# Kernel tuning notes

Hardware: AMD Instinct MI355X
Metric: run time of the kernel (lower is better)

## Reference

```python
import jax, jax.numpy as jnp
import numpy as np

B, C, H, W = 8, 512, 64, 64
IC = C // 2  # inter_channel


def setup_inputs() -> dict:
    key = jax.random.key(0)
    ks = jax.random.split(key, 10)
    s = 0.02
    return {
        "x": jax.random.normal(ks[0], (B, C, H, W), dtype=jnp.float32),
        "y": jax.random.normal(ks[1], (B, C, H, W), dtype=jnp.float32),
        "w_phi": jax.random.normal(ks[2], (IC, C), dtype=jnp.float32) * s,
        "b_phi": jnp.zeros((IC,), dtype=jnp.float32),
        "w_theta": jax.random.normal(ks[3], (IC, C), dtype=jnp.float32) * s,
        "b_theta": jnp.zeros((IC,), dtype=jnp.float32),
        "w_g": jax.random.normal(ks[4], (IC, C), dtype=jnp.float32) * s,
        "b_g": jnp.zeros((IC,), dtype=jnp.float32),
        "w_mask": jax.random.normal(ks[5], (C, IC), dtype=jnp.float32) * s,
        "b_mask": jnp.zeros((C,), dtype=jnp.float32),
    }


def _conv1x1(w, b, t):
    # t: [b, cin, h, w]; 1x1 conv == channel matmul
    return jnp.einsum('oc,bchw->bohw', w, t) + b[None, :, None, None]


def reference(x, y, w_phi, b_phi, w_theta, b_theta, w_g, b_g, w_mask, b_mask):
    b, c, h, w = x.shape
    ic = w_phi.shape[0]  # c // 2
    # Faithful to the torch code: conv outputs ic channels but is viewed as
    # (b, c, -1), so the sequence length is N = h*w//2 and feature dim is c.
    x_phi = _conv1x1(w_phi, b_phi, y).reshape(b, c, -1)              # [b, c, N]
    x_theta = _conv1x1(w_theta, b_theta, x).reshape(b, c, -1)
    x_theta = jnp.transpose(x_theta, (0, 2, 1))                      # [b, N, c]
    x_g = _conv1x1(w_g, b_g, x).reshape(b, c, -1)
    dict
    x_g = jnp.transpose(x_g, (0, 2, 1))                              # [b, N, c]
    scores = jnp.einsum('bnc,bcm->bnm', x_theta, x_phi)              # [b, N, N]
    attn = jax.nn.softmax(scores, axis=1)  # softmax over dim=1 (columns), as in torch
    out_nl = jnp.einsum('bnm,bmc->bnc', attn, x_g)                   # [b, N, c]
    out_nl = jnp.transpose(out_nl, (0, 2, 1)).reshape(b, ic, h, w)   # [b, ic, h, w]
    mask = _conv1x1(w_mask, b_mask, out_nl)                          # [b, c, h, w]
    return mask + x
```

## Files before the change

### kernel.cpp

```cpp
#include <hip/hip_runtime.h>
#include <hip/hip_bf16.h>


typedef __attribute__((ext_vector_type(8))) short short8;
typedef __attribute__((ext_vector_type(4))) short short4v;
typedef __attribute__((ext_vector_type(4))) float f32x4;

__device__ __forceinline__ short f2bf(float f) {
  union { __hip_bfloat16 h; short s; } u; u.h = __float2bfloat16(f); return u.s;
}
__device__ __forceinline__ float bf2f(short s) {
  union { short s; __hip_bfloat16 h; } u; u.s = s; return __bfloat162float(u.h);
}

__device__ __forceinline__ void async_ld16(const void* g, void* l) {
  __builtin_amdgcn_global_load_lds(
      (const __attribute__((address_space(1))) unsigned int*)(unsigned long long)g,
      (__attribute__((address_space(3))) unsigned int*)(unsigned int)(unsigned long long)l,
      16, 0, 0);
}

__device__ __forceinline__ short8 frag_sw(const short* Ds, int row, int q8)
{
  return *(const short8*)&Ds[row * 32 + (((q8 >> 3) ^ ((row >> 2) & 3)) << 3)];
}

__global__ __launch_bounds__(512, 4)
void ov_k(const short* __restrict__ Eg, const short* __restrict__ Gg,
          short* __restrict__ Cg)
{
  const int L = blockIdx.x;
  const int xcd = L & 7, k = L >> 3;
  const int slab = xcd + ((k >> 2) << 3);
  const int bz = slab >> 4, by = slab & 15, bx = k & 3;

  __shared__ __align__(16) short As[128 * 32];
  __shared__ __align__(16) short Bs[128 * 32];
  const short* A = Eg + ((long)bz << 22);
  const short* B = Gg + ((long)bz << 20);
  const int m0 = by * 128;
  const int n0 = bx * 128;
  const int t = threadIdx.x;
  const int wv = t >> 6, ln = t & 63;
  const int wr = wv >> 1, wc = wv & 1;
  const int fr = ln & 15, q8 = (ln >> 4) * 8;
  const int rowA = t >> 2, kc = (t & 3) * 8;

  f32x4 acc[2][4];
  #pragma unroll
  for (int i = 0; i < 2; i++)
    #pragma unroll
    for (int j = 0; j < 4; j++)
      #pragma unroll
      for (int r = 0; r < 4; r++) acc[i][j][r] = 0.f;

  for (int kk = 0; kk < 2048; kk += 32) {
    async_ld16(A + (long)(m0 + rowA) * 2048 + kk + kc, As + wv * 512);
    async_ld16(B + (long)(n0 + rowA) * 2048 + kk + kc, Bs + wv * 512);
    __syncthreads();
    short8 af[2], bfr[4];
    #pragma unroll
    for (int mi = 0; mi < 2; mi++) af[mi] = *(const short8*)&As[(wr * 32 + mi * 16 + fr) * 32 + q8];
    #pragma unroll
    for (int ni = 0; ni < 4; ni++) bfr[ni] = *(const short8*)&Bs[(wc * 64 + ni * 16 + fr) * 32 + q8];
    #pragma unroll
    for (int mi = 0; mi < 2; mi++)
      #pragma unroll
      for (int ni = 0; ni < 4; ni++)
        acc[mi][ni] = __builtin_amdgcn_mfma_f32_16x16x32_bf16(af[mi], bfr[ni], acc[mi][ni], 0, 0, 0);
    __syncthreads();
  }

  const int colb = n0 + wc * 64 + fr;
  const int rowb = m0 + wr * 32 + (ln >> 4) * 4;
  #pragma unroll
  for (int mi = 0; mi < 2; mi++)
    #pragma unroll
    for (int r = 0; r < 4; r++) {
      const int mr = rowb + mi * 16 + r;
      #pragma unroll
      for (int ni = 0; ni < 4; ni++)
        Cg[((long)bz << 20) + (long)mr * 512 + colb + ni * 16] = f2bf(acc[mi][ni][r]);
    }
}

__global__ __launch_bounds__(512, 4)
void conv_ptf(const float* __restrict__ x, const float* __restrict__ y,
              const short* __restrict__ wth, const short* __restrict__ wph,
              const float* __restrict__ bth, const float* __restrict__ bph,
              short* __restrict__ TPT2)
{
  __shared__ __align__(16) short As[2][128 * 32];
  __shared__ __align__(16) short Bs[2][256 * 32];
  const int slab = blockIdx.x;
  const bool isphi = slab >= 256;
  const int s2 = slab & 255;
  const float* src = (isphi ? y : x) + (long)(s2 >> 5) * (512L * 4096);
  const int px0 = (s2 & 31) * 128;
  const long m0 = (long)slab * 128;
  const short* W = isphi ? wph : wth;
  const float* bias = isphi ? bph : bth;
  const int t = threadIdx.x;
  const int wv = t >> 6, ln = t & 63;
  const int wpx = wv >> 2, wic = wv & 3;
  const int fr = ln & 15, q8 = (ln >> 4) * 8;
  const int g4 = (t >> 5) * 4, p4 = (t & 31) * 4;
  const int w2 = wv - 4;

  f32x4 acc[4][4];
  #pragma unroll
  for (int i = 0; i < 4; i++)
    #pragma unroll
    for (int j = 0; j < 4; j++)
      #pragma unroll
      for (int r = 0; r < 4; r++) acc[i][j][r] = 0.f;

  if (t >= 256) {
    #pragma unroll
    for (int j = 0; j < 4; j++)
      async_ld16(W + (long)(w2 * 64 + j * 16 + (ln >> 2)) * 512 + (ln & 3) * 8,
                 &Bs[0][(w2 * 64 + j * 16) * 32]);
  } else {
    f32x4 r[4];
    #pragma unroll
    for (int i = 0; i < 4; i++)
      r[i] = *(const f32x4*)&src[(long)(g4 + i) * 4096 + px0 + p4];
    #pragma unroll
    for (int j = 0; j < 4; j++) {
      short4v w;
      w[0] = f2bf(r[0][j]); w[1] = f2bf(r[1][j]); w[2] = f2bf(r[2][j]); w[3] = f2bf(r[3][j]);
      const int px = p4 + j;
      const int u = (g4 >> 3) ^ ((px >> 2) & 3);
      *(short4v*)&As[0][px * 32 + u * 8 + (g4 & 4)] = w;
    }
  }
  __syncthreads();

  for (int k = 1; k < 16; k++) {
    const int cur = (k - 1) & 1, nxt = k & 1;
    f32x4 r[4];
    if (t >= 256) {
      #pragma unroll
      for (int j = 0; j < 4; j++)
        async_ld16(W + (long)(w2 * 64 + j * 16 + (ln >> 2)) * 512 + k * 32 + (ln & 3) * 8,
                   &Bs[nxt][(w2 * 64 + j * 16) * 32]);
    } else {
      #pragma unroll
      for (int i = 0; i < 4; i++)
        r[i] = *(const f32x4*)&src[(long)(k * 32 + g4 + i) * 4096 + px0 + p4];
    }
    short8 af[4], bfv[4];
    #pragma unroll
    for (int mi = 0; mi < 4; mi++) af[mi] = frag_sw(&As[cur][0], wpx * 64 + mi * 16 + fr, q8);
    #pragma unroll
    for (int ni = 0; ni < 4; ni++) bfv[ni] = *(const short8*)&Bs[cur][(wic * 64 + ni * 16 + fr) * 32 + q8];
    #pragma unroll
    for (int mi = 0; mi < 4; mi++)
      #pragma unroll
      for (int ni = 0; ni < 4; ni++)
        acc[mi][ni] = __builtin_amdgcn_mfma_f32_16x16x32_bf16(af[mi], bfv[ni], acc[mi][ni], 0, 0, 0);
    if (t < 256) {
      #pragma unroll
      for (int j = 0; j < 4; j++) {
        short4v w;
        w[0] = f2bf(r[0][j]); w[1] = f2bf(r[1][j]); w[2] = f2bf(r[2][j]); w[3] = f2bf(r[3][j]);
        const int px = p4 + j;
        const int u = (g4 >> 3) ^ ((px >> 2) & 3);
        *(short4v*)&As[nxt][px * 32 + u * 8 + (g4 & 4)] = w;
      }
    }
    __syncthreads();
  }

  {
    short8 af[4], bfv[4];
    #pragma unroll
    for (int mi = 0; mi < 4; mi++) af[mi] = frag_sw(&As[1][0], wpx * 64 + mi * 16 + fr, q8);
    #pragma unroll
    for (int ni = 0; ni < 4; ni++) bfv[ni] = *(const short8*)&Bs[1][(wic * 64 + ni * 16 + fr) * 32 + q8];
    #pragma unroll
    for (int mi = 0; mi < 4; mi++)
      #pragma unroll
      for (int ni = 0; ni < 4; ni++)
        acc[mi][ni] = __builtin_amdgcn_mfma_f32_16x16x32_bf16(af[mi], bfv[ni], acc[mi][ni], 0, 0, 0);
  }

  const int colic = wic * 64 + fr;
  float cb[4];
  #pragma unroll
  for (int ni = 0; ni < 4; ni++) cb[ni] = bias[colic + ni * 16];
  #pragma unroll
  for (int mi = 0; mi < 4; mi++)
    #pragma unroll
    for (int r = 0; r < 4; r++) {
      const long m = m0 + wpx * 64 + mi * 16 + (ln >> 4) * 4 + r;
      #pragma unroll
      for (int ni = 0; ni < 4; ni++)
        TPT2[m * 256 + colic + ni * 16] = f2bf(acc[mi][ni][r] + cb[ni]);
    }
}

__global__ __launch_bounds__(512, 4)
void gemmG_f(const float* __restrict__ x, const short* __restrict__ wg,
             const float* __restrict__ bg, short* __restrict__ G)
{
  __shared__ __align__(16) short As[2][256 * 32];
  __shared__ __align__(16) short Bs[2][128 * 32];
  const int img = blockIdx.y;
  const int n0 = blockIdx.x * 128;
  const float* src = x + (long)img * 512 * 4096;
  const int t = threadIdx.x;
  const int wv = t >> 6, ln = t & 63;
  const int wr = wv >> 1, wc = wv & 1;
  const int fr = ln & 15, q8 = (ln >> 4) * 8;
  const int g4 = (t >> 5) * 4, p4 = (t & 31) * 4;
  const int w2 = wv - 4;

  f32x4 acc[4][4];
  #pragma unroll
  for (int i = 0; i < 4; i++)
    #pragma unroll
    for (int j = 0; j < 4; j++)
      #pragma unroll
      for (int r = 0; r < 4; r++) acc[i][j][r] = 0.f;

  if (t >= 256) {
    #pragma unroll
    for (int j = 0; j < 4; j++)
      async_ld16(wg + (long)(w2 * 64 + j * 16 + (ln >> 2)) * 512 + (ln & 3) * 8,
                 &As[0][(w2 * 64 + j * 16) * 32]);
  } else {
    f32x4 r[4];
    #pragma unroll
    for (int i = 0; i < 4; i++)
      r[i] = *(const f32x4*)&src[(long)(g4 + i) * 4096 + n0 + p4];
    #pragma unroll
    for (int j = 0; j < 4; j++) {
      short4v w;
      w[0] = f2bf(r[0][j]); w[1] = f2bf(r[1][j]); w[2] = f2bf(r[2][j]); w[3] = f2bf(r[3][j]);
      const int px = p4 + j;
      const int u = (g4 >> 3) ^ ((px >> 2) & 3);
      *(short4v*)&Bs[0][px * 32 + u * 8 + (g4 & 4)] = w;
    }
  }
  __syncthreads();

  for (int k = 1; k < 16; k++) {
    const int cur = (k - 1) & 1, nxt = k & 1;
    f32x4 r[4];
    if (t >= 256) {
      #pragma unroll
      for (int j = 0; j < 4; j++)
        async_ld16(wg + (long)(w2 * 64 + j * 16 + (ln >> 2)) * 512 + k * 32 + (ln & 3) * 8,
                   &As[nxt][(w2 * 64 + j * 16) * 32]);
    } else {
      #pragma unroll
      for (int i = 0; i < 4; i++)
        r[i] = *(const f32x4*)&src[(long)(k * 32 + g4 + i) * 4096 + n0 + p4];
    }
    short8 af[4], bfv[4];
    #pragma unroll
    for (int mi = 0; mi < 4; mi++) af[mi] = *(const short8*)&As[cur][(wr * 64 + mi * 16 + fr) * 32 + q8];
    #pragma unroll
    for (int ni = 0; ni < 4; ni++) bfv[ni] = frag_sw(&Bs[cur][0], wc * 64 + ni * 16 + fr, q8);
    #pragma unroll
    for (int mi = 0; mi < 4; mi++)
      #pragma unroll
      for (int ni = 0; ni < 4; ni++)
        acc[mi][ni] = __builtin_amdgcn_mfma_f32_16x16x32_bf16(af[mi], bfv[ni], acc[mi][ni], 0, 0, 0);
    if (t < 256) {
      #pragma unroll
      for (int j = 0; j < 4; j++) {
        short4v w;
        w[0] = f2bf(r[0][j]); w[1] = f2bf(r[1][j]); w[2] = f2bf(r[2][j]); w[3] = f2bf(r[3][j]);
        const int px = p4 + j;
        const int u = (g4 >> 3) ^ ((px >> 2) & 3);
        *(short4v*)&Bs[nxt][px * 32 + u * 8 + (g4 & 4)] = w;
      }
    }
    __syncthreads();
  }

  {
    short8 af[4], bfv[4];
    #pragma unroll
    for (int mi = 0; mi < 4; mi++) af[mi] = *(const short8*)&As[1][(wr * 64 + mi * 16 + fr) * 32 + q8];
    #pragma unroll
    for (int ni = 0; ni < 4; ni++) bfv[ni] = frag_sw(&Bs[1][0], wc * 64 + ni * 16 + fr, q8);
    #pragma unroll
    for (int mi = 0; mi < 4; mi++)
      #pragma unroll
      for (int ni = 0; ni < 4; ni++)
        acc[mi][ni] = __builtin_amdgcn_mfma_f32_16x16x32_bf16(af[mi], bfv[ni], acc[mi][ni], 0, 0, 0);
  }

  const int colb = n0 + wc * 64 + fr;
  const int rowb = wr * 64 + (ln >> 4) * 4;
  #pragma unroll
  for (int mi = 0; mi < 4; mi++)
    #pragma unroll
    for (int r = 0; r < 4; r++) {
      const int mr = rowb + mi * 16 + r;
      const float badd = bg[mr];
      #pragma unroll
      for (int ni = 0; ni < 4; ni++)
        G[((long)img << 20) + (long)mr * 4096 + colb + ni * 16] = f2bf(acc[mi][ni][r] + badd);
    }
}

__global__ __launch_bounds__(256)
void scores_k(const short* __restrict__ TT2, const short* __restrict__ PT2,
              short* __restrict__ ST, float* __restrict__ pstats)
{
  __shared__ __align__(16) short As[128 * 32];
  __shared__ __align__(16) short Bs[128 * 32];
  const int bz = blockIdx.z, by = blockIdx.y, bx = blockIdx.x;
  const int t = threadIdx.x;
  const int wv = t >> 6, ln = t & 63;
  const int wm = (wv >> 1) * 64, wn = (wv & 1) * 64;
  const int fr = ln & 15, q8 = (ln >> 4) * 8;
  const int rowA = t >> 2, kc = (t & 3) * 8;

  f32x4 acc[4][4];
  #pragma unroll
  for (int i = 0; i < 4; i++)
    #pragma unroll
    for (int j = 0; j < 4; j++)
      #pragma unroll
      for (int r = 0; r < 4; r++) acc[i][j][r] = 0.f;

  #pragma unroll
  for (int h = 0; h < 2; h++) {
    const short* Aseg = TT2 + ((long)(bz * 4096 + h * 2048 + by * 128)) * 256;
    const short* Bseg = PT2 + ((long)(bz * 4096 + h * 2048 + bx * 128)) * 256;
    for (int kk = 0; kk < 256; kk += 32) {
      #pragma unroll
      for (int s = 0; s < 2; s++) {
        async_ld16(Aseg + (long)(s * 64 + rowA) * 256 + kk + kc, As + (s * 256 + wv * 64) * 8);
        async_ld16(Bseg + (long)(s * 64 + rowA) * 256 + kk + kc, Bs + (s * 256 + wv * 64) * 8);
      }
      __syncthreads();
      short8 af[4], bfr[4];
      #pragma unroll
      for (int mi = 0; mi < 4; mi++) af[mi] = *(const short8*)&As[(wm + mi * 16 + fr) * 32 + q8];
      #pragma unroll
      for (int ni = 0; ni < 4; ni++) bfr[ni] = *(const short8*)&Bs[(wn + ni * 16 + fr) * 32 + q8];
      #pragma unroll
      for (int mi = 0; mi < 4; mi++)
        #pragma unroll
        for (int ni = 0; ni < 4; ni++)
          acc[mi][ni] = __builtin_amdgcn_mfma_f32_16x16x32_bf16(af[mi], bfr[ni], acc[mi][ni], 0, 0, 0);
      __syncthreads();
    }
  }

  const int colb = bx * 128 + wn + fr;
  const int rowb = by * 128 + wm + (ln >> 4) * 4;
  short* base = ST + ((long)bz << 22);
  float ps[4] = {0.f, 0.f, 0.f, 0.f};
  #pragma unroll
  for (int mi = 0; mi < 4; mi++)
    #pragma unroll
    for (int r = 0; r < 4; r++) {
      const long mr = rowb + mi * 16 + r;
      #pragma unroll
      for (int ni = 0; ni < 4; ni++) {
        float e = __expf(acc[mi][ni][r]);
        base[mr * 2048 + colb + ni * 16] = f2bf(e);
        ps[ni] += e;
      }
    }
  #pragma unroll
  for (int ni = 0; ni < 4; ni++) {
    ps[ni] += __shfl_xor(ps[ni], 16);
    ps[ni] += __shfl_xor(ps[ni], 32);
  }
  float* part = (float*)As;
  if (ln < 16) {
    #pragma unroll
    for (int ni = 0; ni < 4; ni++)
      part[(wv >> 1) * 128 + wn + ni * 16 + fr] = ps[ni];
  }
  __syncthreads();
  if (t < 128)
    pstats[((long)(bz * 16 + by)) * 2048 + bx * 128 + t] = part[t] + part[128 + t];
}

__global__ __launch_bounds__(256)
void zfinal(const float* __restrict__ pstats, float* __restrict__ invZ)
{
  const int g = blockIdx.x * 256 + threadIdx.x;
  const int b = g >> 11, col = g & 2047;
  float S = 0.f;
  #pragma unroll
  for (int rc = 0; rc < 16; rc++) S += pstats[((long)(b * 16 + rc)) * 2048 + col];
  invZ[g] = 1.f / S;
}

__global__ __launch_bounds__(256)
void g_scale(short* __restrict__ G, const float* __restrict__ invZ)
{
  const long base = ((long)blockIdx.x * 256 + threadIdx.x) * 8;
  const int bz = (int)(base >> 20);
  const int n2 = (int)(base & 4095);
  const float* z = invZ + bz * 2048 + (n2 & 2047);
  short8 v = *(short8*)&G[base];
  f32x4 z0 = *(const f32x4*)z;
  f32x4 z1 = *(const f32x4*)(z + 4);
  #pragma unroll
  for (int j = 0; j < 4; j++) { v[j] = f2bf(bf2f(v[j]) * z0[j]); v[4 + j] = f2bf(bf2f(v[4 + j]) * z1[j]); }
  *(short8*)&G[base] = v;
}

__global__ __launch_bounds__(256)
void mask_k(const short* __restrict__ Wm20, const short* __restrict__ Wm21,
            const short* __restrict__ OVT, const float* __restrict__ bmask,
            const float* __restrict__ x, float* __restrict__ out)
{
  __shared__ __align__(16) short As[128 * 32];
  __shared__ __align__(16) short Bs[128 * 32];
  const int bz = blockIdx.z;
  const int n0 = blockIdx.x * 128;
  const int m0 = blockIdx.y * 128;
  const short* A = (n0 >= 2048) ? Wm21 : Wm20;
  const short* B = OVT + ((long)bz << 20) + (long)(n0 & 2047) * 512;
  const int t = threadIdx.x;
  const int wv = t >> 6, ln = t & 63;
  const int wm = (wv >> 1) * 64, wn = (wv & 1) * 64;
  const int fr = ln & 15, q8 = (ln >> 4) * 8;
  const int rowA = t >> 2, kc = (t & 3) * 8;

  f32x4 acc[4][4];
  #pragma unroll
  for (int i = 0; i < 4; i++)
    #pragma unroll
    for (int j = 0; j < 4; j++)
      #pragma unroll
      for (int r = 0; r < 4; r++) acc[i][j][r] = 0.f;

  for (int kk = 0; kk < 512; kk += 32) {
    #pragma unroll
    for (int s = 0; s < 2; s++) {
      async_ld16(A + (long)(m0 + s * 64 + rowA) * 512 + kk + kc, As + (s * 256 + wv * 64) * 8);
      async_ld16(B + (long)(s * 64 + rowA) * 512 + kk + kc, Bs + (s * 256 + wv * 64) * 8);
    }
    __syncthreads();
    short8 af[4], bfr[4];
    #pragma unroll
    for (int mi = 0; mi < 4; mi++) af[mi] = *(const short8*)&As[(wm + mi * 16 + fr) * 32 + q8];
    #pragma unroll
    for (int ni = 0; ni < 4; ni++) bfr[ni] = *(const short8*)&Bs[(wn + ni * 16 + fr) * 32 + q8];
    #pragma unroll
    for (int mi = 0; mi < 4; mi++)
      #pragma unroll
      for (int ni = 0; ni < 4; ni++)
        acc[mi][ni] = __builtin_amdgcn_mfma_f32_16x16x32_bf16(af[mi], bfr[ni], acc[mi][ni], 0, 0, 0);
    __syncthreads();
  }

  const int colb = n0 + wn + fr;
  const int rowb = m0 + wm + (ln >> 4) * 4;
  #pragma unroll
  for (int mi = 0; mi < 4; mi++)
    #pragma unroll
    for (int r = 0; r < 4; r++) {
      const int mr = rowb + mi * 16 + r;
      const float badd = bmask[mr];
      const long rbase = ((long)bz * 512 + mr) * 4096;
      #pragma unroll
      for (int ni = 0; ni < 4; ni++) {
        const int cc = colb + ni * 16;
        out[rbase + cc] = acc[mi][ni][r] + badd + x[rbase + cc];
      }
    }
}

__global__ __launch_bounds__(256)
void wconv2(const float* w_phi, const float* w_theta, const float* w_g,
            const float* w_mask,
            short* wph, short* wth, short* wg, short* Wm20, short* Wm21)
{
  const int seg = blockIdx.x >> 6;
  const int blk = blockIdx.x & 63;
  const int i0 = blk * 2048 + threadIdx.x * 8;
  if (seg < 3) {
    const float* s = seg == 0 ? w_phi : seg == 1 ? w_theta : w_g;
    short* d = seg == 0 ? wph : seg == 1 ? wth : wg;
    f32x4 a = *(const f32x4*)&s[i0];
    f32x4 b = *(const f32x4*)&s[i0 + 4];
    short8 o;
    #pragma unroll
    for (int j = 0; j < 4; j++) { o[j] = f2bf(a[j]); o[4 + j] = f2bf(b[j]); }
    *(short8*)&d[i0] = o;
  } else {
    const int o = i0 >> 8;
    f32x4 a = *(const f32x4*)&w_mask[i0];
    f32x4 b = *(const f32x4*)&w_mask[i0 + 4];
    short v[8];
    #pragma unroll
    for (int j = 0; j < 4; j++) { v[j] = f2bf(a[j]); v[4 + j] = f2bf(b[j]); }
    short8 a0, a1, b0, b1;
    #pragma unroll
    for (int j = 0; j < 4; j++) {
      a0[2 * j] = v[j];     a0[2 * j + 1] = 0;
      a1[2 * j] = v[4 + j]; a1[2 * j + 1] = 0;
      b0[2 * j] = 0;        b0[2 * j + 1] = v[j];
      b1[2 * j] = 0;        b1[2 * j + 1] = v[4 + j];
    }
    const long base = (long)o * 512 + 2 * (i0 & 255);
    *(short8*)&Wm20[base] = a0; *(short8*)&Wm20[base + 8] = a1;
    *(short8*)&Wm21[base] = b0; *(short8*)&Wm21[base + 8] = b1;
  }
}

extern "C" void kernel_launch(void* const* d_in, const int* in_sizes, int n_in,
                              void* d_out, int out_size, void* d_ws, size_t ws_size,
                              hipStream_t stream)
{
  (void)in_sizes; (void)n_in; (void)out_size; (void)ws_size;
  const float* x       = (const float*)d_in[0];
  const float* y       = (const float*)d_in[1];
  const float* w_phi   = (const float*)d_in[2];
  const float* b_phi   = (const float*)d_in[3];
  const float* w_theta = (const float*)d_in[4];
  const float* b_theta = (const float*)d_in[5];
  const float* w_g     = (const float*)d_in[6];
  const float* b_g     = (const float*)d_in[7];
  const float* w_mask  = (const float*)d_in[8];
  const float* b_mask  = (const float*)d_in[9];
  float* out = (float*)d_out;

  char* ws = (char*)d_ws;
  const long MB = 1L << 20;
  short* wph  = (short*)(ws + 0);
  short* wth  = (short*)(ws + 256 * 1024);
  short* wg   = (short*)(ws + 512 * 1024);
  short* Wm20 = (short*)(ws + 768 * 1024);
  short* Wm21 = (short*)(ws + 1280 * 1024);
  short* TPT2 = (short*)(ws + 66 * MB);
  short* G    = (short*)(ws + 98 * MB);
  short* ST   = (short*)(ws + 2 * MB);
  float* pstats = (float*)(ws + 114 * MB);
  float* invZ   = (float*)(ws + 115 * MB);
  short* OVT  = (short*)(ws + 66 * MB);

  dim3 blk(256, 1, 1);
  dim3 blk8(512, 1, 1);

  wconv2<<<dim3(256, 1, 1), blk, 0, stream>>>(w_phi, w_theta, w_g, w_mask,
                                              wph, wth, wg, Wm20, Wm21);

  conv_ptf<<<dim3(512, 1, 1), blk8, 0, stream>>>(x, y, wth, wph, b_theta, b_phi, TPT2);

  gemmG_f<<<dim3(32, 8, 1), blk8, 0, stream>>>(x, wg, b_g, G);

  scores_k<<<dim3(16, 16, 8), blk, 0, stream>>>(TPT2, TPT2 + 32768L * 256, ST, pstats);
  zfinal<<<dim3(64, 1, 1), blk, 0, stream>>>(pstats, invZ);
  g_scale<<<dim3(4096, 1, 1), blk, 0, stream>>>(G, invZ);

  ov_k<<<dim3(512, 1, 1), blk8, 0, stream>>>(ST, G, OVT);

  mask_k<<<dim3(32, 4, 8), blk, 0, stream>>>(Wm20, Wm21, OVT, b_mask, x, out);
}
```

Baseline: 358.2 us.

## Double-buffer async LDS loads and XOR-swizzle shared-memory tiles across GEMM kernels

Converts the ov_k, scores_k and mask_k main loops from single-buffered load-sync-compute-sync into double-buffered pipelines. The next tile's global_load_lds is issued while MFMAs consume the current tile, which removes one barrier per iteration. It also applies an XOR swizzle to the k-chunk offset on every async LDS load, and reads fragments through frag_sw, to cut LDS bank conflicts, including in the conv/gemmG weight tiles. The cost is twice the LDS footprint in three kernels, which may lower occupancy.

```diff
diff --git a/kernel.cpp b/kernel.cpp
--- a/kernel.cpp
+++ b/kernel.cpp
@@ -34,8 +34,8 @@
   const int slab = xcd + ((k >> 2) << 3);
   const int bz = slab >> 4, by = slab & 15, bx = k & 3;
 
-  __shared__ __align__(16) short As[128 * 32];
-  __shared__ __align__(16) short Bs[128 * 32];
+  __shared__ __align__(16) short As[2][128 * 32];
+  __shared__ __align__(16) short Bs[2][128 * 32];
   const short* A = Eg + ((long)bz << 22);
   const short* B = Gg + ((long)bz << 20);
   const int m0 = by * 128;
@@ -44,7 +44,8 @@
   const int wv = t >> 6, ln = t & 63;
   const int wr = wv >> 1, wc = wv & 1;
   const int fr = ln & 15, q8 = (ln >> 4) * 8;
-  const int rowA = t >> 2, kc = (t & 3) * 8;
+  const int rowA = t >> 2;
+  const int kcs = ((t & 3) ^ ((t >> 4) & 3)) * 8;
 
   f32x4 acc[2][4];
   #pragma unroll
@@ -54,21 +55,37 @@
       #pragma unroll
       for (int r = 0; r < 4; r++) acc[i][j][r] = 0.f;
 
-  for (int kk = 0; kk < 2048; kk += 32) {
-    async_ld16(A + (long)(m0 + rowA) * 2048 + kk + kc, As + wv * 512);
-    async_ld16(B + (long)(n0 + rowA) * 2048 + kk + kc, Bs + wv * 512);
-    __syncthreads();
+  async_ld16(A + (long)(m0 + rowA) * 2048 + kcs, &As[0][0] + wv * 512);
+  async_ld16(B + (long)(n0 + rowA) * 2048 + kcs, &Bs[0][0] + wv * 512);
+  __syncthreads();
+
+  for (int kt = 1; kt < 64; kt++) {
+    const int cur = (kt - 1) & 1, nxt = kt & 1;
+    async_ld16(A + (long)(m0 + rowA) * 2048 + kt * 32 + kcs, &As[nxt][0] + wv * 512);
+    async_ld16(B + (long)(n0 + rowA) * 2048 + kt * 32 + kcs, &Bs[nxt][0] + wv * 512);
     short8 af[2], bfr[4];
     #pragma unroll
-    for (int mi = 0; mi < 2; mi++) af[mi] = *(const short8*)&As[(wr * 32 + mi * 16 + fr) * 32 + q8];
-    #pragma unroll
-    for (int ni = 0; ni < 4; ni++) bfr[ni] = *(const short8*)&Bs[(wc * 64 + ni * 16 + fr) * 32 + q8];
+    for (int mi = 0; mi < 2; mi++) af[mi] = frag_sw(&As[cur][0], wr * 32 + mi * 16 + fr, q8);
+    #pragma unroll
+    for (int ni = 0; ni < 4; ni++) bfr[ni] = frag_sw(&Bs[cur][0], wc * 64 + ni * 16 + fr, q8);
     #pragma unroll
     for (int mi = 0; mi < 2; mi++)
       #pragma unroll
       for (int ni = 0; ni < 4; ni++)
         acc[mi][ni] = __builtin_amdgcn_mfma_f32_16x16x32_bf16(af[mi], bfr[ni], acc[mi][ni], 0, 0, 0);
     __syncthreads();
+  }
+  {
+    short8 af[2], bfr[4];
+    #pragma unroll
+    for (int mi = 0; mi < 2; mi++) af[mi] = frag_sw(&As[1][0], wr * 32 + mi * 16 + fr, q8);
+    #pragma unroll
+    for (int ni = 0; ni < 4; ni++) bfr[ni] = frag_sw(&Bs[1][0], wc * 64 + ni * 16 + fr, q8);
+    #pragma unroll
+    for (int mi = 0; mi < 2; mi++)
+      #pragma unroll
+      for (int ni = 0; ni < 4; ni++)
+        acc[mi][ni] = __builtin_amdgcn_mfma_f32_16x16x32_bf16(af[mi], bfr[ni], acc[mi][ni], 0, 0, 0);
   }
 
   const int colb = n0 + wc * 64 + fr;
@@ -106,6 +123,7 @@
   const int fr = ln & 15, q8 = (ln >> 4) * 8;
   const int g4 = (t >> 5) * 4, p4 = (t & 31) * 4;
   const int w2 = wv - 4;
+  const int kcs = ((ln & 3) ^ (ln >> 4)) * 8;
 
   f32x4 acc[4][4];
   #pragma unroll
@@ -118,7 +136,7 @@
   if (t >= 256) {
     #pragma unroll
     for (int j = 0; j < 4; j++)
-      async_ld16(W + (long)(w2 * 64 + j * 16 + (ln >> 2)) * 512 + (ln & 3) * 8,
+      async_ld16(W + (long)(w2 * 64 + j * 16 + (ln >> 2)) * 512 + kcs,
                  &Bs[0][(w2 * 64 + j * 16) * 32]);
   } else {
     f32x4 r[4];
@@ -142,7 +160,7 @@
     if (t >= 256) {
       #pragma unroll
       for (int j = 0; j < 4; j++)
-        async_ld16(W + (long)(w2 * 64 + j * 16 + (ln >> 2)) * 512 + k * 32 + (ln & 3) * 8,
+        async_ld16(W + (long)(w2 * 64 + j * 16 + (ln >> 2)) * 512 + k * 32 + kcs,
                    &Bs[nxt][(w2 * 64 + j * 16) * 32]);
     } else {
       #pragma unroll
@@ -153,7 +171,7 @@
     #pragma unroll
     for (int mi = 0; mi < 4; mi++) af[mi] = frag_sw(&As[cur][0], wpx * 64 + mi * 16 + fr, q8);
     #pragma unroll
-    for (int ni = 0; ni < 4; ni++) bfv[ni] = *(const short8*)&Bs[cur][(wic * 64 + ni * 16 + fr) * 32 + q8];
+    for (int ni = 0; ni < 4; ni++) bfv[ni] = frag_sw(&Bs[cur][0], wic * 64 + ni * 16 + fr, q8);
     #pragma unroll
     for (int mi = 0; mi < 4; mi++)
       #pragma unroll
@@ -177,7 +195,7 @@
     #pragma unroll
     for (int mi = 0; mi < 4; mi++) af[mi] = frag_sw(&As[1][0], wpx * 64 + mi * 16 + fr, q8);
     #pragma unroll
-    for (int ni = 0; ni < 4; ni++) bfv[ni] = *(const short8*)&Bs[1][(wic * 64 + ni * 16 + fr) * 32 + q8];
+    for (int ni = 0; ni < 4; ni++) bfv[ni] = frag_sw(&Bs[1][0], wic * 64 + ni * 16 + fr, q8);
     #pragma unroll
     for (int mi = 0; mi < 4; mi++)
       #pragma unroll
@@ -215,6 +233,7 @@
   const int fr = ln & 15, q8 = (ln >> 4) * 8;
   const int g4 = (t >> 5) * 4, p4 = (t & 31) * 4;
   const int w2 = wv - 4;
+  const int kcs = ((ln & 3) ^ (ln >> 4)) * 8;
 
   f32x4 acc[4][4];
   #pragma unroll
@@ -227,7 +246,7 @@
   if (t >= 256) {
     #pragma unroll
     for (int j = 0; j < 4; j++)
-      async_ld16(wg + (long)(w2 * 64 + j * 16 + (ln >> 2)) * 512 + (ln & 3) * 8,
+      async_ld16(wg + (long)(w2 * 64 + j * 16 + (ln >> 2)) * 512 + kcs,
                  &As[0][(w2 * 64 + j * 16) * 32]);
   } else {
     f32x4 r[4];
@@ -251,7 +270,7 @@
     if (t >= 256) {
       #pragma unroll
       for (int j = 0; j < 4; j++)
-        async_ld16(wg + (long)(w2 * 64 + j * 16 + (ln >> 2)) * 512 + k * 32 + (ln & 3) * 8,
+        async_ld16(wg + (long)(w2 * 64 + j * 16 + (ln >> 2)) * 512 + k * 32 + kcs,
                    &As[nxt][(w2 * 64 + j * 16) * 32]);
     } else {
       #pragma unroll
@@ -260,7 +279,7 @@
     }
     short8 af[4], bfv[4];
     #pragma unroll
-    for (int mi = 0; mi < 4; mi++) af[mi] = *(const short8*)&As[cur][(wr * 64 + mi * 16 + fr) * 32 + q8];
+    for (int mi = 0; mi < 4; mi++) af[mi] = frag_sw(&As[cur][0], wr * 64 + mi * 16 + fr, q8);
     #pragma unroll
     for (int ni = 0; ni < 4; ni++) bfv[ni] = frag_sw(&Bs[cur][0], wc * 64 + ni * 16 + fr, q8);
     #pragma unroll
@@ -284,7 +303,7 @@
   {
     short8 af[4], bfv[4];
     #pragma unroll
-    for (int mi = 0; mi < 4; mi++) af[mi] = *(const short8*)&As[1][(wr * 64 + mi * 16 + fr) * 32 + q8];
+    for (int mi = 0; mi < 4; mi++) af[mi] = frag_sw(&As[1][0], wr * 64 + mi * 16 + fr, q8);
     #pragma unroll
     for (int ni = 0; ni < 4; ni++) bfv[ni] = frag_sw(&Bs[1][0], wc * 64 + ni * 16 + fr, q8);
     #pragma unroll
@@ -312,14 +331,18 @@
 void scores_k(const short* __restrict__ TT2, const short* __restrict__ PT2,
               short* __restrict__ ST, float* __restrict__ pstats)
 {
-  __shared__ __align__(16) short As[128 * 32];
-  __shared__ __align__(16) short Bs[128 * 32];
+  __shared__ __align__(16) short As[2][128 * 32];
+  __shared__ __align__(16) short Bs[2][128 * 32];
   const int bz = blockIdx.z, by = blockIdx.y, bx = blockIdx.x;
   const int t = threadIdx.x;
   const int wv = t >> 6, ln = t & 63;
   const int wm = (wv >> 1) * 64, wn = (wv & 1) * 64;
   const int fr = ln & 15, q8 = (ln >> 4) * 8;
-  const int rowA = t >> 2, kc = (t & 3) * 8;
+  const int rowA = t >> 2;
+  const int kcs = ((t & 3) ^ ((t >> 4) & 3)) * 8;
+
+  const short* Abase = TT2 + ((long)(bz * 4096 + by * 128)) * 256;
+  const short* Bbase = PT2 + ((long)(bz * 4096 + bx * 128)) * 256;
 
   f32x4 acc[4][4];
   #pragma unroll
@@ -329,30 +352,49 @@
       #pragma unroll
       for (int r = 0; r < 4; r++) acc[i][j][r] = 0.f;
 
-  #pragma unroll
-  for (int h = 0; h < 2; h++) {
-    const short* Aseg = TT2 + ((long)(bz * 4096 + h * 2048 + by * 128)) * 256;
-    const short* Bseg = PT2 + ((long)(bz * 4096 + h * 2048 + bx * 128)) * 256;
-    for (int kk = 0; kk < 256; kk += 32) {
-      #pragma unroll
-      for (int s = 0; s < 2; s++) {
-        async_ld16(Aseg + (long)(s * 64 + rowA) * 256 + kk + kc, As + (s * 256 + wv * 64) * 8);
-        async_ld16(Bseg + (long)(s * 64 + rowA) * 256 + kk + kc, Bs + (s * 256 + wv * 64) * 8);
-      }
-      __syncthreads();
-      short8 af[4], bfr[4];
-      #pragma unroll
-      for (int mi = 0; mi < 4; mi++) af[mi] = *(const short8*)&As[(wm + mi * 16 + fr) * 32 + q8];
-      #pragma unroll
-      for (int ni = 0; ni < 4; ni++) bfr[ni] = *(const short8*)&Bs[(wn + ni * 16 + fr) * 32 + q8];
-      #pragma unroll
-      for (int mi = 0; mi < 4; mi++)
-        #pragma unroll
-        for (int ni = 0; ni < 4; ni++)
-          acc[mi][ni] = __builtin_amdgcn_mfma_f32_16x16x32_bf16(af[mi], bfr[ni], acc[mi][ni], 0, 0, 0);
-      __syncthreads();
-    }
-  }
+  #define SC_STAGE(s, buf)                                                     \
+    {                                                                          \
+      const long hoff = (long)((s) >> 3) * 2048 * 256;                         \
+      const int kk = ((s) & 7) * 32;                                           \
+      _Pragma("unroll")                                                        \
+      for (int sv = 0; sv < 2; sv++) {                                         \
+        async_ld16(Abase + hoff + (long)(sv * 64 + rowA) * 256 + kk + kcs,     \
+                   &As[buf][0] + (sv * 256 + wv * 64) * 8);                    \
+        async_ld16(Bbase + hoff + (long)(sv * 64 + rowA) * 256 + kk + kcs,     \
+                   &Bs[buf][0] + (sv * 256 + wv * 64) * 8);                    \
+      }                                                                        \
+    }
+
+  SC_STAGE(0, 0);
+  __syncthreads();
+  for (int s = 1; s < 16; s++) {
+    const int cur = (s - 1) & 1, nxt = s & 1;
+    SC_STAGE(s, nxt);
+    short8 af[4], bfr[4];
+    #pragma unroll
+    for (int mi = 0; mi < 4; mi++) af[mi] = frag_sw(&As[cur][0], wm + mi * 16 + fr, q8);
+    #pragma unroll
+    for (int ni = 0; ni < 4; ni++) bfr[ni] = frag_sw(&Bs[cur][0], wn + ni * 16 + fr, q8);
+    #pragma unroll
+    for (int mi = 0; mi < 4; mi++)
+      #pragma unroll
+      for (int ni = 0; ni < 4; ni++)
+        acc[mi][ni] = __builtin_amdgcn_mfma_f32_16x16x32_bf16(af[mi], bfr[ni], acc[mi][ni], 0, 0, 0);
+    __syncthreads();
+  }
+  {
+    short8 af[4], bfr[4];
+    #pragma unroll
+    for (int mi = 0; mi < 4; mi++) af[mi] = frag_sw(&As[1][0], wm + mi * 16 + fr, q8);
+    #pragma unroll
+    for (int ni = 0; ni < 4; ni++) bfr[ni] = frag_sw(&Bs[1][0], wn + ni * 16 + fr, q8);
+    #pragma unroll
+    for (int mi = 0; mi < 4; mi++)
+      #pragma unroll
+      for (int ni = 0; ni < 4; ni++)
+        acc[mi][ni] = __builtin_amdgcn_mfma_f32_16x16x32_bf16(af[mi], bfr[ni], acc[mi][ni], 0, 0, 0);
+  }
+  #undef SC_STAGE
 
   const int colb = bx * 128 + wn + fr;
   const int rowb = by * 128 + wm + (ln >> 4) * 4;
@@ -375,7 +417,7 @@
     ps[ni] += __shfl_xor(ps[ni], 16);
     ps[ni] += __shfl_xor(ps[ni], 32);
   }
-  float* part = (float*)As;
+  float* part = (float*)&As[0][0];
   if (ln < 16) {
     #pragma unroll
     for (int ni = 0; ni < 4; ni++)
@@ -417,8 +459,8 @@
             const short* __restrict__ OVT, const float* __restrict__ bmask,
             const float* __restrict__ x, float* __restrict__ out)
 {
-  __shared__ __align__(16) short As[128 * 32];
-  __shared__ __align__(16) short Bs[128 * 32];
+  __shared__ __align__(16) short As[2][128 * 32];
+  __shared__ __align__(16) short Bs[2][128 * 32];
   const int bz = blockIdx.z;
   const int n0 = blockIdx.x * 128;
   const int m0 = blockIdx.y * 128;
@@ -428,7 +470,8 @@
   const int wv = t >> 6, ln = t & 63;
   const int wm = (wv >> 1) * 64, wn = (wv & 1) * 64;
   const int fr = ln & 15, q8 = (ln >> 4) * 8;
-  const int rowA = t >> 2, kc = (t & 3) * 8;
+  const int rowA = t >> 2;
+  const int kcs = ((t & 3) ^ ((t >> 4) & 3)) * 8;
 
   f32x4 acc[4][4];
   #pragma unroll
@@ -438,18 +481,28 @@
       #pragma unroll
       for (int r = 0; r < 4; r++) acc[i][j][r] = 0.f;
 
-  for (int kk = 0; kk < 512; kk += 32) {
-    #pragma unroll
-    for (int s = 0; s < 2; s++) {
-      async_ld16(A + (long)(m0 + s * 64 + rowA) * 512 + kk + kc, As + (s * 256 + wv * 64) * 8);
-      async_ld16(B + (long)(s * 64 + rowA) * 512 + kk + kc, Bs + (s * 256 + wv * 64) * 8);
-    }
-    __syncthreads();
+  #define MK_STAGE(s, buf)                                                     \
+    {                                                                          \
+      const int kk = (s) * 32;                                                 \
+      _Pragma("unroll")                                                        \
+      for (int sv = 0; sv < 2; sv++) {                                         \
+        async_ld16(A + (long)(m0 + sv * 64 + rowA) * 512 + kk + kcs,           \
+                   &As[buf][0] + (sv * 256 + wv * 64) * 8);                    \
+        async_ld16(B + (long)(sv * 64 + rowA) * 512 + kk + kcs,                \
+                   &Bs[buf][0] + (sv * 256 + wv * 64) * 8);                    \
+      }                                                                        \
+    }
+
+  MK_STAGE(0, 0);
+  __syncthreads();
+  for (int s = 1; s < 16; s++) {
+    const int cur = (s - 1) & 1, nxt = s & 1;
+    MK_STAGE(s, nxt);
     short8 af[4], bfr[4];
     #pragma unroll
-    for (int mi = 0; mi < 4; mi++) af[mi] = *(const short8*)&As[(wm + mi * 16 + fr) * 32 + q8];
-    #pragma unroll
-    for (int ni = 0; ni < 4; ni++) bfr[ni] = *(const short8*)&Bs[(wn + ni * 16 + fr) * 32 + q8];
+    for (int mi = 0; mi < 4; mi++) af[mi] = frag_sw(&As[cur][0], wm + mi * 16 + fr, q8);
+    #pragma unroll
+    for (int ni = 0; ni < 4; ni++) bfr[ni] = frag_sw(&Bs[cur][0], wn + ni * 16 + fr, q8);
     #pragma unroll
     for (int mi = 0; mi < 4; mi++)
       #pragma unroll
@@ -457,6 +510,19 @@
         acc[mi][ni] = __builtin_amdgcn_mfma_f32_16x16x32_bf16(af[mi], bfr[ni], acc[mi][ni], 0, 0, 0);
     __syncthreads();
   }
+  {
+    short8 af[4], bfr[4];
+    #pragma unroll
+    for (int mi = 0; mi < 4; mi++) af[mi] = frag_sw(&As[1][0], wm + mi * 16 + fr, q8);
+    #pragma unroll
+    for (int ni = 0; ni < 4; ni++) bfr[ni] = frag_sw(&Bs[1][0], wn + ni * 16 + fr, q8);
+    #pragma unroll
+    for (int mi = 0; mi < 4; mi++)
+      #pragma unroll
+      for (int ni = 0; ni < 4; ni++)
+        acc[mi][ni] = __builtin_amdgcn_mfma_f32_16x16x32_bf16(af[mi], bfr[ni], acc[mi][ni], 0, 0, 0);
+  }
+  #undef MK_STAGE
 
   const int colb = n0 + wn + fr;
   const int rowb = m0 + wm + (ln >> 4) * 4;
```

Result: no change. 361.4 us (+0.9%).
